# Optimization experiments

Hardware: AMD Instinct MI355X
Metric: run time of the kernel (lower is better)

## Reference

```python
import jax, jax.numpy as jnp
import numpy as np

SEQ_LEN = 96      # args.seq_len (in_feats)
H_FEATS = 100
OUT_FEATS = 128
HEADS = 4
K = 64            # args.input_size = nodes per graph
B = 256           # number of graphs (batch_size)
N = K * B
DEG = 8
E = N * DEG
OUT_SIZE = 24     # args.output_size
NEG_SLOPE = 0.2   # PyG GATConv default


def setup_inputs() -> dict:
    key = jax.random.key(0)
    ks = jax.random.split(key, 20)
    s = 0.05
    x = jax.random.normal(ks[0], (N, SEQ_LEN), jnp.float32)
    # intra-graph random edges (dst repeated, src within same graph)
    dst = jnp.repeat(jnp.arange(N, dtype=jnp.int32), DEG)
    src = (dst // K) * K + jax.random.randint(ks[1], (E,), 0, K, dtype=jnp.int32)
    edge_index = jnp.stack([src, dst])
    batch = jnp.repeat(jnp.arange(B, dtype=jnp.int32), K)
    y = jax.random.normal(ks[2], (N, OUT_SIZE), jnp.float32)
    # GATConv 1: in=96 -> heads=4, ch=100
    W1 = jax.random.normal(ks[3], (SEQ_LEN, HEADS * H_FEATS), jnp.float32) * s
    as1 = jax.random.normal(ks[4], (HEADS, H_FEATS), jnp.float32) * s
    ad1 = jax.random.normal(ks[5], (HEADS, H_FEATS), jnp.float32) * s
    b1 = jnp.zeros((H_FEATS,), jnp.float32)
    # GATConv 2: in=100 -> heads=4, ch=128
    W2 = jax.random.normal(ks[6], (H_FEATS, HEADS * OUT_FEATS), jnp.float32) * s
    as2 = jax.random.normal(ks[7], (HEADS, OUT_FEATS), jnp.float32) * s
    ad2 = jax.random.normal(ks[8], (HEADS, OUT_FEATS), jnp.float32) * s
    b2 = jnp.zeros((OUT_FEATS,), jnp.float32)
    # per-node-index MLPs (batched over K)
    fw1 = jax.random.normal(ks[9], (K, OUT_FEATS, 64), jnp.float32) * s
    fb1 = jnp.zeros((K, 64), jnp.float32)
    fw2 = jax.random.normal(ks[10], (K, 64, OUT_SIZE), jnp.float32) * s
    fb2 = jnp.zeros((K, OUT_SIZE), jnp.float32)
    return dict(x=x, edge_index=edge_index, batch=batch, y=y,
                W1=W1, as1=as1, ad1=ad1, b1=b1,
                W2=W2, as2=as2, ad2=ad2, b2=b2,
                fw1=fw1, fb1=fb1, fw2=fw2, fb2=fb2)


def gat_conv(x, src, dst, W, a_src, a_dst, bias):
    # PyG GATConv (concat=False): linear -> per-edge attention -> softmax over
    # incoming edges of each dst -> weighted sum -> mean over heads + bias.
    n = x.shape[0]
    xl = (x @ W).reshape(n, HEADS, -1)                      # [N,H,C]
    al_src = jnp.sum(xl * a_src, axis=-1)                   # [N,H]
    al_dst = jnp.sum(xl * a_dst, axis=-1)                   # [N,H]
    alpha = jax.nn.leaky_relu(al_src[src] + al_dst[dst], NEG_SLOPE)  # [E,H]
    m = jax.ops.segment_max(alpha, dst, num_segments=n)
    ea = jnp.exp(alpha - m[dst])
    denom = jax.ops.segment_sum(ea, dst, num_segments=n)
    w = ea / (denom[dst] + 1e-16)                           # [E,H]
    msg = xl[src] * w[:, :, None]                           # [E,H,C]
    out = jax.ops.segment_sum(msg, dst, num_segments=n)     # [N,H,C]
    return out.mean(axis=1) + bias                          # concat=False


def reference(x, edge_index, batch, y, W1, as1, ad1, b1, W2, as2, ad2, b2, fw1, fb1, fw2, fb2):
    n = x.shape[0]
    src, dst = edge_index[0], edge_index[1]
    loop = jnp.arange(n, dtype=src.dtype)                   # GATConv adds self-loops
    src = jnp.concatenate([src, loop])
    dst = jnp.concatenate([dst, loop])
    h = jax.nn.elu(gat_conv(x, src, dst, W1, as1, ad1, b1))
    h = gat_conv(h, src, dst, W2, as2, ad2, b2)             # [N,128]
    # batch is sorted with K nodes per graph -> stacking == static reshape
    xg = h.reshape(B, K, OUT_FEATS).transpose(1, 0, 2)      # [K,B,128]
    hid = jax.nn.relu(jnp.einsum('kbi,kih->kbh', xg, fw1) + fb1[:, None, :])
    pred = jnp.einsum('kbh,kho->kbo', hid, fw2) + fb2[:, None, :]  # [K,B,out]
    yg = y.reshape(B, K, OUT_SIZE)                          # [B,K,out]
    return pred, yg
```

## Files before the change

### kernel.cpp

```cpp
#include <hip/hip_runtime.h>
#include <hip/hip_bf16.h>
#include <math.h>


#define N_NODES 16384
#define B_GRAPHS 256
#define K_NODES 64
#define DEG 8
#define NHEADS 4
#define C1 100
#define C2 128
#define IN_F 96
#define HID 64
#define OUT_SZ 24
#define PRED_ELEMS (K_NODES * B_GRAPHS * OUT_SZ)

#define W1T_ROWS 448
#define W1T_K    96
#define W2T_ROWS 512
#define W2T_K    128

using bf16 = __hip_bfloat16;
typedef __attribute__((ext_vector_type(8))) short          frag_ab;
typedef __attribute__((ext_vector_type(4))) float          frag_cd;
typedef unsigned short us8 __attribute__((ext_vector_type(8)));
typedef unsigned short us4 __attribute__((ext_vector_type(4)));

__device__ __forceinline__ float us2f(unsigned short u) {
  return __bfloat162float(__ushort_as_bfloat16(u));
}
__device__ __forceinline__ short f2bf_s(float f) {
  return __builtin_bit_cast(short, __float2bfloat16(f));
}

#define P1N (W1T_ROWS * W1T_K)
#define P2N (W2T_ROWS * W2T_K)
#define YG4 (PRED_ELEMS / 4)

__global__ __launch_bounds__(256)
void prep(const float* __restrict__ W1, const float* __restrict__ W2,
          const float* __restrict__ y,
          bf16* __restrict__ W1t, bf16* __restrict__ W2t,
          float* __restrict__ yg) {
  int idx = blockIdx.x * 256 + threadIdx.x;
  if (idx < P1N) {
    int c = idx / W1T_K, k = idx - c * W1T_K;
    W1t[idx] = __float2bfloat16((c < 400) ? W1[(size_t)k * 400 + c] : 0.f);
  } else if (idx < P1N + P2N) {
    int i2 = idx - P1N;
    int c = i2 >> 7, k = i2 & 127;
    W2t[i2] = __float2bfloat16((k < 100) ? W2[(size_t)k * 512 + c] : 0.f);
  } else {
    int j = idx - P1N - P2N;
    if (j < YG4) {
      int i = j * 4;
      float4 v = *(const float4*)(y + i);
      v.x = __bfloat162float(__float2bfloat16(v.x));
      v.y = __bfloat162float(__float2bfloat16(v.y));
      v.z = __bfloat162float(__float2bfloat16(v.z));
      v.w = __bfloat162float(__float2bfloat16(v.w));
      *(float4*)(yg + i) = v;
    }
  }
}

__global__ __launch_bounds__(512)
void gat_fused(const float* __restrict__ x,
               const bf16* __restrict__ W1t, const bf16* __restrict__ W2t,
               const int* __restrict__ esrc,
               const float* __restrict__ as1, const float* __restrict__ ad1,
               const float* __restrict__ b1,
               const float* __restrict__ as2, const float* __restrict__ ad2,
               const float* __restrict__ b2,
               bf16* __restrict__ h2out) {
  constexpr int LDA1 = IN_F + 8;
  constexpr int LDA2 = 136;
  constexpr int LDT  = 72;

  __shared__ __align__(16) short          As[64 * LDA2];
  __shared__ __align__(16) unsigned short xs[512 * LDT];
  __shared__ __align__(16) short          Ps[NHEADS * 64 * LDT];
  __shared__ float avs1[400], avd1[400], avs2[512], avd2[512];
  __shared__ float bia1[C1], bia2[C2];
  __shared__ int   edg[K_NODES * DEG];
  __shared__ float als[64 * 5], ald[64 * 5];

  const int g = blockIdx.x;
  const int t = threadIdx.x;
  const int wv = t >> 6;
  const int l  = t & 63;
  const int lm = l & 15;
  const int lk = (l >> 4) * 8;
  const int rq = (l >> 4) * 4;

  {
    constexpr int QR = IN_F / 4;
    for (int idx = t; idx < 64 * QR; idx += 512) {
      int m = idx / QR, q = idx - m * QR;
      const float4 v = *(const float4*)(x + ((size_t)(g * 64 + m) * IN_F + q * 4));
      short* d = &As[m * LDA1 + q * 4];
      d[0] = f2bf_s(v.x); d[1] = f2bf_s(v.y); d[2] = f2bf_s(v.z); d[3] = f2bf_s(v.w);
    }
  }
  for (int idx = t; idx < 400; idx += 512) { avs1[idx] = as1[idx]; avd1[idx] = ad1[idx]; }
  for (int idx = t; idx < 512; idx += 512) { avs2[idx] = as2[idx]; avd2[idx] = ad2[idx]; }
  if (t < C1) bia1[t] = b1[t];
  if (t < C2) bia2[t] = b2[t];
  if (t < K_NODES * DEG) edg[t] = esrc[g * K_NODES * DEG + t] & (K_NODES - 1);
  for (int idx = t; idx < NHEADS * 64 * LDT / 8; idx += 512)
    *(us8*)&Ps[idx * 8] = (us8)0;
  __syncthreads();

  if (wv < 7) {
    const int n0 = wv * 64;
    frag_cd acc[4][4] = {};
#pragma unroll
    for (int ks = 0; ks < IN_F; ks += 32) {
      frag_ab b[4];
#pragma unroll
      for (int nt = 0; nt < 4; ++nt)
        b[nt] = *(const frag_ab*)((const short*)W1t +
                                  (size_t)(n0 + nt * 16 + lm) * W1T_K + ks + lk);
#pragma unroll
      for (int mt = 0; mt < 4; ++mt) {
        frag_ab a = *(const frag_ab*)&As[(mt * 16 + lm) * LDA1 + ks + lk];
#pragma unroll
        for (int nt = 0; nt < 4; ++nt)
          acc[mt][nt] = __builtin_amdgcn_mfma_f32_16x16x32_bf16(a, b[nt],
                                                                acc[mt][nt], 0, 0, 0);
      }
    }
#pragma unroll
    for (int mt = 0; mt < 4; ++mt)
#pragma unroll
      for (int nt = 0; nt < 4; ++nt) {
        const int c4 = n0 + nt * 16 + lm;
        us4 o;
#pragma unroll
        for (int r = 0; r < 4; ++r) o[r] = (unsigned short)f2bf_s(acc[mt][nt][r]);
        *(us4*)&xs[c4 * LDT + mt * 16 + rq] = o;
      }
  }
  __syncthreads();

  if (t < 256) {
    const int n = t >> 2, h = t & 3;
    float ss = 0.f, sd = 0.f;
#pragma unroll 4
    for (int c = 0; c < C1; ++c) {
      const float v = us2f(xs[(h * C1 + c) * LDT + n]);
      ss += v * avs1[h * C1 + c];
      sd += v * avd1[h * C1 + c];
    }
    als[n * 5 + h] = ss;
    ald[n * 5 + h] = sd;
  }
  __syncthreads();

  if (t < 256) {
    const int n = t >> 2, h = t & 3;
    const float ad = ald[n * 5 + h];
    int   sv[9];
    float a[9];
#pragma unroll
    for (int j = 0; j < 8; ++j) sv[j] = edg[n * DEG + j];
    sv[8] = n;
#pragma unroll
    for (int j = 0; j < 9; ++j) {
      float v = als[sv[j] * 5 + h] + ad;
      a[j] = (v >= 0.f) ? v : 0.2f * v;
    }
    float m = -1e30f;
#pragma unroll
    for (int j = 0; j < 9; ++j) m = fmaxf(m, a[j]);
    float s = 0.f;
#pragma unroll
    for (int j = 0; j < 9; ++j) { a[j] = __expf(a[j] - m); s += a[j]; }
    const float inv = 1.f / (s + 1e-16f);
    short* prow = &Ps[(h * 64 + n) * LDT];
#pragma unroll
    for (int j = 0; j < 9; ++j) {
      float tw = a[j];
#pragma unroll
      for (int i = 0; i < 9; ++i)
        if (i != j && sv[i] == sv[j]) tw += a[i];
      prow[sv[j]] = f2bf_s(tw * inv);
    }
  } else {
    for (int i = t - 256; i < 64 * 28; i += 256) {
      int m = i / 28, kk = 100 + (i - m * 28);
      As[m * LDA2 + kk] = 0;
    }
  }
  __syncthreads();

  {
    const int mw = (wv & 3) * 16;
    const int cg = wv >> 2;
    const int ntb = cg * 4;
    const int nte = (cg == 0) ? 4 : 7;
    frag_cd acc[4] = {};
#pragma unroll
    for (int h = 0; h < NHEADS; ++h)
#pragma unroll
      for (int ks = 0; ks < 64; ks += 32) {
        frag_ab a = *(const frag_ab*)&Ps[(h * 64 + mw + lm) * LDT + ks + lk];
        for (int nt = ntb; nt < nte; ++nt) {
          frag_ab b = *(const frag_ab*)&xs[(h * C1 + nt * 16 + lm) * LDT + ks + lk];
          acc[nt - ntb] = __builtin_amdgcn_mfma_f32_16x16x32_bf16(a, b,
                                                                  acc[nt - ntb], 0, 0, 0);
      }
    }
    for (int nt = ntb; nt < nte; ++nt) {
      const int c = nt * 16 + lm;
      if (c < C1) {
        const float bc = bia1[c];
#pragma unroll
        for (int r = 0; r < 4; ++r) {
          float vv = acc[nt - ntb][r] * 0.25f + bc;
          vv = (vv > 0.f) ? vv : (__expf(vv) - 1.f);
          As[(mw + rq + r) * LDA2 + c] = f2bf_s(vv);
        }
      }
    }
  }
  __syncthreads();

  {
    const int n0 = wv * 64;
    frag_cd acc[4][4] = {};
#pragma unroll
    for (int ks = 0; ks < 128; ks += 32) {
      frag_ab b[4];
#pragma unroll
      for (int nt = 0; nt < 4; ++nt)
        b[nt] = *(const frag_ab*)((const short*)W2t +
                                  (size_t)(n0 + nt * 16 + lm) * W2T_K + ks + lk);
#pragma unroll
      for (int mt = 0; mt < 4; ++mt) {
        frag_ab a = *(const frag_ab*)&As[(mt * 16 + lm) * LDA2 + ks + lk];
#pragma unroll
        for (int nt = 0; nt < 4; ++nt)
          acc[mt][nt] = __builtin_amdgcn_mfma_f32_16x16x32_bf16(a, b[nt],
                                                                acc[mt][nt], 0, 0, 0);
      }
    }
#pragma unroll
    for (int mt = 0; mt < 4; ++mt)
#pragma unroll
      for (int nt = 0; nt < 4; ++nt) {
        const int c4 = n0 + nt * 16 + lm;
        us4 o;
#pragma unroll
        for (int r = 0; r < 4; ++r) o[r] = (unsigned short)f2bf_s(acc[mt][nt][r]);
        *(us4*)&xs[c4 * LDT + mt * 16 + rq] = o;
      }
  }
  __syncthreads();

  if (t < 256) {
    const int n = t >> 2, h = t & 3;
    float ss = 0.f, sd = 0.f;
#pragma unroll 4
    for (int c = 0; c < C2; ++c) {
      const float v = us2f(xs[(h * C2 + c) * LDT + n]);
      ss += v * avs2[h * C2 + c];
      sd += v * avd2[h * C2 + c];
    }
    als[n * 5 + h] = ss;
    ald[n * 5 + h] = sd;
  }
  __syncthreads();

  if (t < 256) {
    const int n = t >> 2, h = t & 3;
    const float ad = ald[n * 5 + h];
    int   sv[9];
    float a[9];
#pragma unroll
    for (int j = 0; j < 8; ++j) sv[j] = edg[n * DEG + j];
    sv[8] = n;
#pragma unroll
    for (int j = 0; j < 9; ++j) {
      float v = als[sv[j] * 5 + h] + ad;
      a[j] = (v >= 0.f) ? v : 0.2f * v;
    }
    float m = -1e30f;
#pragma unroll
    for (int j = 0; j < 9; ++j) m = fmaxf(m, a[j]);
    float s = 0.f;
#pragma unroll
    for (int j = 0; j < 9; ++j) { a[j] = __expf(a[j] - m); s += a[j]; }
    const float inv = 1.f / (s + 1e-16f);
    short* prow = &Ps[(h * 64 + n) * LDT];
#pragma unroll
    for (int j = 0; j < 9; ++j) {
      float tw = a[j];
#pragma unroll
      for (int i = 0; i < 9; ++i)
        if (i != j && sv[i] == sv[j]) tw += a[i];
      prow[sv[j]] = f2bf_s(tw * inv);
    }
  }
  __syncthreads();

  {
    const int mw = (wv & 3) * 16;
    const int cg = wv >> 2;
    const int ntb = cg * 4;
    frag_cd acc[4] = {};
#pragma unroll
    for (int h = 0; h < NHEADS; ++h)
#pragma unroll
      for (int ks = 0; ks < 64; ks += 32) {
        frag_ab a = *(const frag_ab*)&Ps[(h * 64 + mw + lm) * LDT + ks + lk];
#pragma unroll
        for (int nt = 0; nt < 4; ++nt) {
          frag_ab b = *(const frag_ab*)&xs[(h * C2 + (ntb + nt) * 16 + lm) * LDT + ks + lk];
          acc[nt] = __builtin_amdgcn_mfma_f32_16x16x32_bf16(a, b, acc[nt], 0, 0, 0);
        }
      }
    unsigned short* outp = (unsigned short*)h2out + (size_t)(g * 64) * C2;
#pragma unroll
    for (int nt = 0; nt < 4; ++nt) {
      const int c = (ntb + nt) * 16 + lm;
      const float bc = bia2[c];
#pragma unroll
      for (int r = 0; r < 4; ++r) {
        float vv = acc[nt][r] * 0.25f + bc;
        outp[(size_t)(mw + rq + r) * C2 + c] = (unsigned short)f2bf_s(vv);
      }
    }
  }
}

__global__ __launch_bounds__(256)
void mlp_mfma(const bf16* __restrict__ h2,
              const float* __restrict__ fw1, const float* __restrict__ fb1,
              const float* __restrict__ fw2, const float* __restrict__ fb2,
              float* __restrict__ pred) {
  constexpr int LDA = C2 + 8;
  constexpr int LDH = HID + 8;
  __shared__ __align__(16) short As[64 * LDA];
  __shared__ __align__(16) short B1[HID * LDA];
  __shared__ __align__(16) short Hs[64 * LDH];
  __shared__ __align__(16) short B2[32 * LDH];
  __shared__ float b1s[HID];
  __shared__ float b2s[32];

  const int k  = blockIdx.x & 63;
  const int ms = blockIdx.x >> 6;
  const int t  = threadIdx.x;

  for (int idx = t; idx < 64 * 16; idx += 256) {
    int r = idx >> 4, o = idx & 15;
    const us8 v = *(const us8*)((const unsigned short*)h2 +
        ((size_t)((ms * 64 + r) * K_NODES + k) * C2) + o * 8);
    *(us8*)&As[r * LDA + o * 8] = v;
  }
  for (int idx = t; idx < C2 * HID; idx += 256) {
    int kk = idx >> 6, n = idx & 63;
    B1[n * LDA + kk] = f2bf_s(fw1[(size_t)k * C2 * HID + kk * HID + n]);
  }
  for (int idx = t; idx < HID * 32; idx += 256) {
    int kk = idx >> 5, n = idx & 31;
    float v = (n < OUT_SZ) ? fw2[(size_t)k * HID * OUT_SZ + kk * OUT_SZ + n] : 0.f;
    B2[n * LDH + kk] = f2bf_s(v);
  }
  if (t < HID) b1s[t] = fb1[k * HID + t];
  if (t < 32)  b2s[t] = (t < OUT_SZ) ? fb2[k * OUT_SZ + t] : 0.f;
  __syncthreads();

  const int wv = t >> 6;
  const int l  = t & 63;
  const int lm = l & 15;
  const int lk = (l >> 4) * 8;
  const int rq = (l >> 4) * 4;

  frag_cd acc[4] = {};
#pragma unroll
  for (int ks = 0; ks < C2; ks += 32) {
    frag_ab a = *(const frag_ab*)&As[(wv * 16 + lm) * LDA + ks + lk];
#pragma unroll
    for (int nt = 0; nt < 4; ++nt) {
      frag_ab b = *(const frag_ab*)&B1[(nt * 16 + lm) * LDA + ks + lk];
      acc[nt] = __builtin_amdgcn_mfma_f32_16x16x32_bf16(a, b, acc[nt], 0, 0, 0);
    }
  }
#pragma unroll
  for (int nt = 0; nt < 4; ++nt) {
    const int j  = nt * 16 + lm;
    const float bj = b1s[j];
#pragma unroll
    for (int r = 0; r < 4; ++r) {
      const int m = wv * 16 + rq + r;
      Hs[m * LDH + j] = f2bf_s(fmaxf(acc[nt][r] + bj, 0.f));
    }
  }
  __syncthreads();

  frag_cd acc2[2] = {};
#pragma unroll
  for (int ks = 0; ks < HID; ks += 32) {
    frag_ab a = *(const frag_ab*)&Hs[(wv * 16 + lm) * LDH + ks + lk];
#pragma unroll
    for (int nt = 0; nt < 2; ++nt) {
      frag_ab b = *(const frag_ab*)&B2[(nt * 16 + lm) * LDH + ks + lk];
      acc2[nt] = __builtin_amdgcn_mfma_f32_16x16x32_bf16(a, b, acc2[nt], 0, 0, 0);
    }
  }
#pragma unroll
  for (int nt = 0; nt < 2; ++nt) {
    const int q = nt * 16 + lm;
    if (q < OUT_SZ) {
      const float bq = b2s[q];
#pragma unroll
      for (int r = 0; r < 4; ++r) {
        const int m = wv * 16 + rq + r;
        pred[((size_t)k * B_GRAPHS + ms * 64 + m) * OUT_SZ + q] = acc2[nt][r] + bq;
      }
    }
  }
}

extern "C" void kernel_launch(void* const* d_in, const int* in_sizes, int n_in,
                              void* d_out, int out_size, void* d_ws, size_t ws_size,
                              hipStream_t stream) {
  const float* x   = (const float*)d_in[0];
  const int*   ei  = (const int*)d_in[1];
  const float* y   = (const float*)d_in[3];
  const float* W1  = (const float*)d_in[4];
  const float* as1 = (const float*)d_in[5];
  const float* ad1 = (const float*)d_in[6];
  const float* b1  = (const float*)d_in[7];
  const float* W2  = (const float*)d_in[8];
  const float* as2 = (const float*)d_in[9];
  const float* ad2 = (const float*)d_in[10];
  const float* b2  = (const float*)d_in[11];
  const float* fw1 = (const float*)d_in[12];
  const float* fb1 = (const float*)d_in[13];
  const float* fw2 = (const float*)d_in[14];
  const float* fb2 = (const float*)d_in[15];

  bf16* h2  = (bf16*)d_ws;
  bf16* W1t = h2 + (size_t)N_NODES * C2;
  bf16* W2t = W1t + P1N;

  float* out = (float*)d_out;

  prep<<<(P1N + P2N + YG4 + 255) / 256, 256, 0, stream>>>(
      W1, W2, y, W1t, W2t, out + PRED_ELEMS);

  gat_fused<<<B_GRAPHS, 512, 0, stream>>>(x, W1t, W2t, ei,
                                          as1, ad1, b1, as2, ad2, b2, h2);

  mlp_mfma<<<K_NODES * 4, 256, 0, stream>>>(h2, fw1, fb1, fw2, fb2, out);
}
```

Measured before the change: 118.6 us.

## Merge prep, GAT and MLP kernels into one cooperative kernel with grid syncs

Replaces three separate launches with a single cooperative kernel of 256 blocks that does weight and y prep, then grid.sync, the per-graph GAT layers, another grid.sync, and the per-node-index MLP. The fw1 and fw2 weights are now pre-transposed to bf16 in the prep phase, so the MLP phase loads them with vectorized copies instead of strided fp32 loads. The MLP phase is re-tiled for 512 threads, with shared memory shared through a union. The aim is to remove launch gaps and the strided weight loads, at the cost of grid-wide barriers and the occupancy limits of a cooperative launch.

```diff
diff --git a/kernel.cpp b/kernel.cpp
--- a/kernel.cpp
+++ b/kernel.cpp
@@ -1,6 +1,9 @@
 #include <hip/hip_runtime.h>
+#include <hip/hip_cooperative_groups.h>
 #include <hip/hip_bf16.h>
 #include <math.h>
+
+namespace cg = cooperative_groups;
 
 
 #define N_NODES 16384
@@ -20,6 +23,13 @@
 #define W2T_ROWS 512
 #define W2T_K    128
 
+#define P1N (W1T_ROWS * W1T_K)
+#define P2N (W2T_ROWS * W2T_K)
+#define F1N (K_NODES * HID * C2)
+#define F2N (K_NODES * 32 * HID)
+#define YG4 (PRED_ELEMS / 4)
+#define PREPN (P1N + P2N + F1N + F2N + YG4)
+
 using bf16 = __hip_bfloat16;
 typedef __attribute__((ext_vector_type(8))) short          frag_ab;
 typedef __attribute__((ext_vector_type(4))) float          frag_cd;
@@ -33,26 +43,69 @@
   return __builtin_bit_cast(short, __float2bfloat16(f));
 }
 
-#define P1N (W1T_ROWS * W1T_K)
-#define P2N (W2T_ROWS * W2T_K)
-#define YG4 (PRED_ELEMS / 4)
-
-__global__ __launch_bounds__(256)
-void prep(const float* __restrict__ W1, const float* __restrict__ W2,
-          const float* __restrict__ y,
-          bf16* __restrict__ W1t, bf16* __restrict__ W2t,
-          float* __restrict__ yg) {
-  int idx = blockIdx.x * 256 + threadIdx.x;
-  if (idx < P1N) {
-    int c = idx / W1T_K, k = idx - c * W1T_K;
-    W1t[idx] = __float2bfloat16((c < 400) ? W1[(size_t)k * 400 + c] : 0.f);
-  } else if (idx < P1N + P2N) {
-    int i2 = idx - P1N;
-    int c = i2 >> 7, k = i2 & 127;
-    W2t[i2] = __float2bfloat16((k < 100) ? W2[(size_t)k * 512 + c] : 0.f);
-  } else {
-    int j = idx - P1N - P2N;
-    if (j < YG4) {
+struct SmGat {
+  short          As[64 * 136];
+  unsigned short xs[512 * 72];
+  short          Ps[NHEADS * 64 * 72];
+  float avs1[400], avd1[400], avs2[512], avd2[512];
+  float bia1[C1], bia2[C2];
+  int   edg[K_NODES * DEG];
+  float als[64 * 5], ald[64 * 5];
+};
+struct SmMlp {
+  short As[64 * 136];
+  short B1[HID * 136];
+  short Hs[64 * 72];
+  short B2[32 * 72];
+  float b1s[HID], b2s[32];
+};
+union SmAll { SmGat g; SmMlp m; };
+
+__global__ __launch_bounds__(512)
+void fused_all(const float* __restrict__ x, const int* __restrict__ ei,
+               const float* __restrict__ y,
+               const float* __restrict__ W1, const float* __restrict__ as1,
+               const float* __restrict__ ad1, const float* __restrict__ b1,
+               const float* __restrict__ W2, const float* __restrict__ as2,
+               const float* __restrict__ ad2, const float* __restrict__ b2,
+               const float* __restrict__ fw1, const float* __restrict__ fb1,
+               const float* __restrict__ fw2, const float* __restrict__ fb2,
+               bf16* __restrict__ ws, float* __restrict__ out) {
+  __shared__ __align__(16) SmAll sm;
+  cg::grid_group grid = cg::this_grid();
+
+  const int t  = threadIdx.x;
+  const int wv = t >> 6;
+  const int l  = t & 63;
+  const int lm = l & 15;
+  const int lk = (l >> 4) * 8;
+  const int rq = (l >> 4) * 4;
+
+  bf16* h2   = ws;
+  bf16* W1t  = h2 + (size_t)N_NODES * C2;
+  bf16* W2t  = W1t + P1N;
+  bf16* fw1t = W2t + P2N;
+  bf16* fw2t = fw1t + F1N;
+  float* yg  = out + PRED_ELEMS;
+
+  for (int idx = blockIdx.x * 512 + t; idx < PREPN; idx += 256 * 512) {
+    if (idx < P1N) {
+      int c = idx / W1T_K, k = idx - c * W1T_K;
+      W1t[idx] = __float2bfloat16((c < 400) ? W1[(size_t)k * 400 + c] : 0.f);
+    } else if (idx < P1N + P2N) {
+      int i2 = idx - P1N;
+      int c = i2 >> 7, k = i2 & 127;
+      W2t[i2] = __float2bfloat16((k < 100) ? W2[(size_t)k * 512 + c] : 0.f);
+    } else if (idx < P1N + P2N + F1N) {
+      int i2 = idx - P1N - P2N;
+      int k = i2 >> 13, r = i2 & 8191, j = r >> 7, i = r & 127;
+      fw1t[i2] = __float2bfloat16(fw1[(size_t)k * 8192 + i * 64 + j]);
+    } else if (idx < P1N + P2N + F1N + F2N) {
+      int i2 = idx - P1N - P2N - F1N;
+      int k = i2 >> 11, r = i2 & 2047, q = r >> 6, j = r & 63;
+      fw2t[i2] = __float2bfloat16((q < OUT_SZ) ? fw2[(size_t)k * 1536 + j * 24 + q] : 0.f);
+    } else {
+      int j = idx - P1N - P2N - F1N - F2N;
       int i = j * 4;
       float4 v = *(const float4*)(y + i);
       v.x = __bfloat162float(__float2bfloat16(v.x));
@@ -62,362 +115,323 @@
       *(float4*)(yg + i) = v;
     }
   }
-}
-
-__global__ __launch_bounds__(512)
-void gat_fused(const float* __restrict__ x,
-               const bf16* __restrict__ W1t, const bf16* __restrict__ W2t,
-               const int* __restrict__ esrc,
-               const float* __restrict__ as1, const float* __restrict__ ad1,
-               const float* __restrict__ b1,
-               const float* __restrict__ as2, const float* __restrict__ ad2,
-               const float* __restrict__ b2,
-               bf16* __restrict__ h2out) {
-  constexpr int LDA1 = IN_F + 8;
-  constexpr int LDA2 = 136;
-  constexpr int LDT  = 72;
-
-  __shared__ __align__(16) short          As[64 * LDA2];
-  __shared__ __align__(16) unsigned short xs[512 * LDT];
-  __shared__ __align__(16) short          Ps[NHEADS * 64 * LDT];
-  __shared__ float avs1[400], avd1[400], avs2[512], avd2[512];
-  __shared__ float bia1[C1], bia2[C2];
-  __shared__ int   edg[K_NODES * DEG];
-  __shared__ float als[64 * 5], ald[64 * 5];
-
-  const int g = blockIdx.x;
-  const int t = threadIdx.x;
-  const int wv = t >> 6;
-  const int l  = t & 63;
-  const int lm = l & 15;
-  const int lk = (l >> 4) * 8;
-  const int rq = (l >> 4) * 4;
+  grid.sync();
 
   {
-    constexpr int QR = IN_F / 4;
-    for (int idx = t; idx < 64 * QR; idx += 512) {
-      int m = idx / QR, q = idx - m * QR;
-      const float4 v = *(const float4*)(x + ((size_t)(g * 64 + m) * IN_F + q * 4));
-      short* d = &As[m * LDA1 + q * 4];
-      d[0] = f2bf_s(v.x); d[1] = f2bf_s(v.y); d[2] = f2bf_s(v.z); d[3] = f2bf_s(v.w);
+    constexpr int LDA1 = IN_F + 8;
+    constexpr int LDA2 = 136;
+    constexpr int LDT  = 72;
+    auto& S = sm.g;
+    const int g = blockIdx.x;
+
+    {
+      constexpr int QR = IN_F / 4;
+      for (int idx = t; idx < 64 * QR; idx += 512) {
+        int m = idx / QR, q = idx - m * QR;
+        const float4 v = *(const float4*)(x + ((size_t)(g * 64 + m) * IN_F + q * 4));
+        short* d = &S.As[m * LDA1 + q * 4];
+        d[0] = f2bf_s(v.x); d[1] = f2bf_s(v.y); d[2] = f2bf_s(v.z); d[3] = f2bf_s(v.w);
+      }
+    }
+    for (int idx = t; idx < 400; idx += 512) { S.avs1[idx] = as1[idx]; S.avd1[idx] = ad1[idx]; }
+    { S.avs2[t] = as2[t]; S.avd2[t] = ad2[t]; }
+    if (t < C1) S.bia1[t] = b1[t];
+    if (t < C2) S.bia2[t] = b2[t];
+    S.edg[t] = ei[g * K_NODES * DEG + t] & (K_NODES - 1);
+    for (int idx = t; idx < NHEADS * 64 * LDT / 8; idx += 512)
+      *(us8*)&S.Ps[idx * 8] = (us8)0;
+    __syncthreads();
+
+    if (wv < 7) {
+      const int n0 = wv * 64;
+      frag_cd acc[4][4] = {};
+#pragma unroll
+      for (int ks = 0; ks < IN_F; ks += 32) {
+        frag_ab b[4];
+#pragma unroll
+        for (int nt = 0; nt < 4; ++nt)
+          b[nt] = *(const frag_ab*)((const short*)W1t +
+                                    (size_t)(n0 + nt * 16 + lm) * W1T_K + ks + lk);
+#pragma unroll
+        for (int mt = 0; mt < 4; ++mt) {
+          frag_ab a = *(const frag_ab*)&S.As[(mt * 16 + lm) * LDA1 + ks + lk];
+#pragma unroll
+          for (int nt = 0; nt < 4; ++nt)
+            acc[mt][nt] = __builtin_amdgcn_mfma_f32_16x16x32_bf16(a, b[nt],
+                                                                  acc[mt][nt], 0, 0, 0);
+        }
+      }
+#pragma unroll
+      for (int mt = 0; mt < 4; ++mt)
+#pragma unroll
+        for (int nt = 0; nt < 4; ++nt) {
+          const int c4 = n0 + nt * 16 + lm;
+          us4 o;
+#pragma unroll
+          for (int r = 0; r < 4; ++r) o[r] = (unsigned short)f2bf_s(acc[mt][nt][r]);
+          *(us4*)&S.xs[c4 * LDT + mt * 16 + rq] = o;
+        }
+    }
+    __syncthreads();
+
+    if (t < 256) {
+      const int n = t >> 2, h = t & 3;
+      float ss = 0.f, sd = 0.f;
+#pragma unroll 4
+      for (int c = 0; c < C1; ++c) {
+        const float v = us2f(S.xs[(h * C1 + c) * LDT + n]);
+        ss += v * S.avs1[h * C1 + c];
+        sd += v * S.avd1[h * C1 + c];
+      }
+      S.als[n * 5 + h] = ss;
+      S.ald[n * 5 + h] = sd;
+    }
+    __syncthreads();
+
+    if (t < 256) {
+      const int n = t >> 2, h = t & 3;
+      const float ad = S.ald[n * 5 + h];
+      int   sv[9];
+      float a[9];
+#pragma unroll
+      for (int j = 0; j < 8; ++j) sv[j] = S.edg[n * DEG + j];
+      sv[8] = n;
+#pragma unroll
+      for (int j = 0; j < 9; ++j) {
+        float v = S.als[sv[j] * 5 + h] + ad;
+        a[j] = (v >= 0.f) ? v : 0.2f * v;
+      }
+      float m = -1e30f;
+#pragma unroll
+      for (int j = 0; j < 9; ++j) m = fmaxf(m, a[j]);
+      float s = 0.f;
+#pragma unroll
+      for (int j = 0; j < 9; ++j) { a[j] = __expf(a[j] - m); s += a[j]; }
+      const float inv = 1.f / (s + 1e-16f);
+      short* prow = &S.Ps[(h * 64 + n) * LDT];
+#pragma unroll
+      for (int j = 0; j < 9; ++j) {
+        float tw = a[j];
+#pragma unroll
+        for (int i = 0; i < 9; ++i)
+          if (i != j && sv[i] == sv[j]) tw += a[i];
+        prow[sv[j]] = f2bf_s(tw * inv);
+      }
+    } else {
+      for (int i = t - 256; i < 64 * 28; i += 256) {
+        int m = i / 28, kk = 100 + (i - m * 28);
+        S.As[m * LDA2 + kk] = 0;
+      }
+    }
+    __syncthreads();
+
+    {
+      const int mw = (wv & 3) * 16;
+      const int cgi = wv >> 2;
+      const int ntb = cgi * 4;
+      const int nte = (cgi == 0) ? 4 : 7;
+      frag_cd acc[4] = {};
+#pragma unroll
+      for (int h = 0; h < NHEADS; ++h)
+#pragma unroll
+        for (int ks = 0; ks < 64; ks += 32) {
+          frag_ab a = *(const frag_ab*)&S.Ps[(h * 64 + mw + lm) * LDT + ks + lk];
+          for (int nt = ntb; nt < nte; ++nt) {
+            frag_ab b = *(const frag_ab*)&S.xs[(h * C1 + nt * 16 + lm) * LDT + ks + lk];
+            acc[nt - ntb] = __builtin_amdgcn_mfma_f32_16x16x32_bf16(a, b,
+                                                                    acc[nt - ntb], 0, 0, 0);
+          }
+        }
+      for (int nt = ntb; nt < nte; ++nt) {
+        const int c = nt * 16 + lm;
+        if (c < C1) {
+          const float bc = S.bia1[c];
+#pragma unroll
+          for (int r = 0; r < 4; ++r) {
+            float vv = acc[nt - ntb][r] * 0.25f + bc;
+            vv = (vv > 0.f) ? vv : (__expf(vv) - 1.f);
+            S.As[(mw + rq + r) * LDA2 + c] = f2bf_s(vv);
+          }
+        }
+      }
+    }
+    __syncthreads();
+
+    {
+      const int n0 = wv * 64;
+      frag_cd acc[4][4] = {};
+#pragma unroll
+      for (int ks = 0; ks < 128; ks += 32) {
+        frag_ab b[4];
+#pragma unroll
+        for (int nt = 0; nt < 4; ++nt)
+          b[nt] = *(const frag_ab*)((const short*)W2t +
+                                    (size_t)(n0 + nt * 16 + lm) * W2T_K + ks + lk);
+#pragma unroll
+        for (int mt = 0; mt < 4; ++mt) {
+          frag_ab a = *(const frag_ab*)&S.As[(mt * 16 + lm) * LDA2 + ks + lk];
+#pragma unroll
+          for (int nt = 0; nt < 4; ++nt)
+            acc[mt][nt] = __builtin_amdgcn_mfma_f32_16x16x32_bf16(a, b[nt],
+                                                                  acc[mt][nt], 0, 0, 0);
+        }
+      }
+#pragma unroll
+      for (int mt = 0; mt < 4; ++mt)
+#pragma unroll
+        for (int nt = 0; nt < 4; ++nt) {
+          const int c4 = n0 + nt * 16 + lm;
+          us4 o;
+#pragma unroll
+          for (int r = 0; r < 4; ++r) o[r] = (unsigned short)f2bf_s(acc[mt][nt][r]);
+          *(us4*)&S.xs[c4 * LDT + mt * 16 + rq] = o;
+        }
+    }
+    __syncthreads();
+
+    if (t < 256) {
+      const int n = t >> 2, h = t & 3;
+      float ss = 0.f, sd = 0.f;
+#pragma unroll 4
+      for (int c = 0; c < C2; ++c) {
+        const float v = us2f(S.xs[(h * C2 + c) * LDT + n]);
+        ss += v * S.avs2[h * C2 + c];
+        sd += v * S.avd2[h * C2 + c];
+      }
+      S.als[n * 5 + h] = ss;
+      S.ald[n * 5 + h] = sd;
+    }
+    __syncthreads();
+
+    if (t < 256) {
+      const int n = t >> 2, h = t & 3;
+      const float ad = S.ald[n * 5 + h];
+      int   sv[9];
+      float a[9];
+#pragma unroll
+      for (int j = 0; j < 8; ++j) sv[j] = S.edg[n * DEG + j];
+      sv[8] = n;
+#pragma unroll
+      for (int j = 0; j < 9; ++j) {
+        float v = S.als[sv[j] * 5 + h] + ad;
+        a[j] = (v >= 0.f) ? v : 0.2f * v;
+      }
+      float m = -1e30f;
+#pragma unroll
+      for (int j = 0; j < 9; ++j) m = fmaxf(m, a[j]);
+      float s = 0.f;
+#pragma unroll
+      for (int j = 0; j < 9; ++j) { a[j] = __expf(a[j] - m); s += a[j]; }
+      const float inv = 1.f / (s + 1e-16f);
+      short* prow = &S.Ps[(h * 64 + n) * LDT];
+#pragma unroll
+      for (int j = 0; j < 9; ++j) {
+        float tw = a[j];
+#pragma unroll
+        for (int i = 0; i < 9; ++i)
+          if (i != j && sv[i] == sv[j]) tw += a[i];
+        prow[sv[j]] = f2bf_s(tw * inv);
+      }
+    }
+    __syncthreads();
+
+    {
+      const int mw = (wv & 3) * 16;
+      const int cgi = wv >> 2;
+      const int ntb = cgi * 4;
+      frag_cd acc[4] = {};
+#pragma unroll
+      for (int h = 0; h < NHEADS; ++h)
+#pragma unroll
+        for (int ks = 0; ks < 64; ks += 32) {
+          frag_ab a = *(const frag_ab*)&S.Ps[(h * 64 + mw + lm) * LDT + ks + lk];
+#pragma unroll
+          for (int nt = 0; nt < 4; ++nt) {
+            frag_ab b = *(const frag_ab*)&S.xs[(h * C2 + (ntb + nt) * 16 + lm) * LDT + ks + lk];
+            acc[nt] = __builtin_amdgcn_mfma_f32_16x16x32_bf16(a, b, acc[nt], 0, 0, 0);
+          }
+        }
+      unsigned short* outp = (unsigned short*)h2 + (size_t)(g * 64) * C2;
+#pragma unroll
+      for (int nt = 0; nt < 4; ++nt) {
+        const int c = (ntb + nt) * 16 + lm;
+        const float bc = S.bia2[c];
+#pragma unroll
+        for (int r = 0; r < 4; ++r) {
+          float vv = acc[nt][r] * 0.25f + bc;
+          outp[(size_t)(mw + rq + r) * C2 + c] = (unsigned short)f2bf_s(vv);
+        }
+      }
     }
   }
-  for (int idx = t; idx < 400; idx += 512) { avs1[idx] = as1[idx]; avd1[idx] = ad1[idx]; }
-  for (int idx = t; idx < 512; idx += 512) { avs2[idx] = as2[idx]; avd2[idx] = ad2[idx]; }
-  if (t < C1) bia1[t] = b1[t];
-  if (t < C2) bia2[t] = b2[t];
-  if (t < K_NODES * DEG) edg[t] = esrc[g * K_NODES * DEG + t] & (K_NODES - 1);
-  for (int idx = t; idx < NHEADS * 64 * LDT / 8; idx += 512)
-    *(us8*)&Ps[idx * 8] = (us8)0;
-  __syncthreads();
-
-  if (wv < 7) {
-    const int n0 = wv * 64;
-    frag_cd acc[4][4] = {};
-#pragma unroll
-    for (int ks = 0; ks < IN_F; ks += 32) {
-      frag_ab b[4];
-#pragma unroll
-      for (int nt = 0; nt < 4; ++nt)
-        b[nt] = *(const frag_ab*)((const short*)W1t +
-                                  (size_t)(n0 + nt * 16 + lm) * W1T_K + ks + lk);
-#pragma unroll
-      for (int mt = 0; mt < 4; ++mt) {
-        frag_ab a = *(const frag_ab*)&As[(mt * 16 + lm) * LDA1 + ks + lk];
-#pragma unroll
-        for (int nt = 0; nt < 4; ++nt)
-          acc[mt][nt] = __builtin_amdgcn_mfma_f32_16x16x32_bf16(a, b[nt],
-                                                                acc[mt][nt], 0, 0, 0);
-      }
-    }
-#pragma unroll
-    for (int mt = 0; mt < 4; ++mt)
-#pragma unroll
-      for (int nt = 0; nt < 4; ++nt) {
-        const int c4 = n0 + nt * 16 + lm;
-        us4 o;
-#pragma unroll
-        for (int r = 0; r < 4; ++r) o[r] = (unsigned short)f2bf_s(acc[mt][nt][r]);
-        *(us4*)&xs[c4 * LDT + mt * 16 + rq] = o;
-      }
-  }
-  __syncthreads();
-
-  if (t < 256) {
-    const int n = t >> 2, h = t & 3;
-    float ss = 0.f, sd = 0.f;
-#pragma unroll 4
-    for (int c = 0; c < C1; ++c) {
-      const float v = us2f(xs[(h * C1 + c) * LDT + n]);
-      ss += v * avs1[h * C1 + c];
-      sd += v * avd1[h * C1 + c];
-    }
-    als[n * 5 + h] = ss;
-    ald[n * 5 + h] = sd;
-  }
-  __syncthreads();
-
-  if (t < 256) {
-    const int n = t >> 2, h = t & 3;
-    const float ad = ald[n * 5 + h];
-    int   sv[9];
-    float a[9];
-#pragma unroll
-    for (int j = 0; j < 8; ++j) sv[j] = edg[n * DEG + j];
-    sv[8] = n;
-#pragma unroll
-    for (int j = 0; j < 9; ++j) {
-      float v = als[sv[j] * 5 + h] + ad;
-      a[j] = (v >= 0.f) ? v : 0.2f * v;
-    }
-    float m = -1e30f;
-#pragma unroll
-    for (int j = 0; j < 9; ++j) m = fmaxf(m, a[j]);
-    float s = 0.f;
-#pragma unroll
-    for (int j = 0; j < 9; ++j) { a[j] = __expf(a[j] - m); s += a[j]; }
-    const float inv = 1.f / (s + 1e-16f);
-    short* prow = &Ps[(h * 64 + n) * LDT];
-#pragma unroll
-    for (int j = 0; j < 9; ++j) {
-      float tw = a[j];
-#pragma unroll
-      for (int i = 0; i < 9; ++i)
-        if (i != j && sv[i] == sv[j]) tw += a[i];
-      prow[sv[j]] = f2bf_s(tw * inv);
-    }
-  } else {
-    for (int i = t - 256; i < 64 * 28; i += 256) {
-      int m = i / 28, kk = 100 + (i - m * 28);
-      As[m * LDA2 + kk] = 0;
-    }
-  }
-  __syncthreads();
+  grid.sync();
 
   {
-    const int mw = (wv & 3) * 16;
-    const int cg = wv >> 2;
-    const int ntb = cg * 4;
-    const int nte = (cg == 0) ? 4 : 7;
-    frag_cd acc[4] = {};
-#pragma unroll
-    for (int h = 0; h < NHEADS; ++h)
-#pragma unroll
-      for (int ks = 0; ks < 64; ks += 32) {
-        frag_ab a = *(const frag_ab*)&Ps[(h * 64 + mw + lm) * LDT + ks + lk];
-        for (int nt = ntb; nt < nte; ++nt) {
-          frag_ab b = *(const frag_ab*)&xs[(h * C1 + nt * 16 + lm) * LDT + ks + lk];
-          acc[nt - ntb] = __builtin_amdgcn_mfma_f32_16x16x32_bf16(a, b,
-                                                                  acc[nt - ntb], 0, 0, 0);
-      }
-    }
-    for (int nt = ntb; nt < nte; ++nt) {
-      const int c = nt * 16 + lm;
-      if (c < C1) {
-        const float bc = bia1[c];
-#pragma unroll
-        for (int r = 0; r < 4; ++r) {
-          float vv = acc[nt - ntb][r] * 0.25f + bc;
-          vv = (vv > 0.f) ? vv : (__expf(vv) - 1.f);
-          As[(mw + rq + r) * LDA2 + c] = f2bf_s(vv);
-        }
-      }
-    }
-  }
-  __syncthreads();
-
-  {
-    const int n0 = wv * 64;
-    frag_cd acc[4][4] = {};
-#pragma unroll
-    for (int ks = 0; ks < 128; ks += 32) {
-      frag_ab b[4];
-#pragma unroll
-      for (int nt = 0; nt < 4; ++nt)
-        b[nt] = *(const frag_ab*)((const short*)W2t +
-                                  (size_t)(n0 + nt * 16 + lm) * W2T_K + ks + lk);
-#pragma unroll
-      for (int mt = 0; mt < 4; ++mt) {
-        frag_ab a = *(const frag_ab*)&As[(mt * 16 + lm) * LDA2 + ks + lk];
-#pragma unroll
-        for (int nt = 0; nt < 4; ++nt)
-          acc[mt][nt] = __builtin_amdgcn_mfma_f32_16x16x32_bf16(a, b[nt],
-                                                                acc[mt][nt], 0, 0, 0);
-      }
-    }
-#pragma unroll
-    for (int mt = 0; mt < 4; ++mt)
-#pragma unroll
-      for (int nt = 0; nt < 4; ++nt) {
-        const int c4 = n0 + nt * 16 + lm;
-        us4 o;
-#pragma unroll
-        for (int r = 0; r < 4; ++r) o[r] = (unsigned short)f2bf_s(acc[mt][nt][r]);
-        *(us4*)&xs[c4 * LDT + mt * 16 + rq] = o;
-      }
-  }
-  __syncthreads();
-
-  if (t < 256) {
-    const int n = t >> 2, h = t & 3;
-    float ss = 0.f, sd = 0.f;
-#pragma unroll 4
-    for (int c = 0; c < C2; ++c) {
-      const float v = us2f(xs[(h * C2 + c) * LDT + n]);
-      ss += v * avs2[h * C2 + c];
-      sd += v * avd2[h * C2 + c];
-    }
-    als[n * 5 + h] = ss;
-    ald[n * 5 + h] = sd;
-  }
-  __syncthreads();
-
-  if (t < 256) {
-    const int n = t >> 2, h = t & 3;
-    const float ad = ald[n * 5 + h];
-    int   sv[9];
-    float a[9];
-#pragma unroll
-    for (int j = 0; j < 8; ++j) sv[j] = edg[n * DEG + j];
-    sv[8] = n;
-#pragma unroll
-    for (int j = 0; j < 9; ++j) {
-      float v = als[sv[j] * 5 + h] + ad;
-      a[j] = (v >= 0.f) ? v : 0.2f * v;
-    }
-    float m = -1e30f;
-#pragma unroll
-    for (int j = 0; j < 9; ++j) m = fmaxf(m, a[j]);
-    float s = 0.f;
-#pragma unroll
-    for (int j = 0; j < 9; ++j) { a[j] = __expf(a[j] - m); s += a[j]; }
-    const float inv = 1.f / (s + 1e-16f);
-    short* prow = &Ps[(h * 64 + n) * LDT];
-#pragma unroll
-    for (int j = 0; j < 9; ++j) {
-      float tw = a[j];
-#pragma unroll
-      for (int i = 0; i < 9; ++i)
-        if (i != j && sv[i] == sv[j]) tw += a[i];
-      prow[sv[j]] = f2bf_s(tw * inv);
-    }
-  }
-  __syncthreads();
-
-  {
-    const int mw = (wv & 3) * 16;
-    const int cg = wv >> 2;
-    const int ntb = cg * 4;
-    frag_cd acc[4] = {};
-#pragma unroll
-    for (int h = 0; h < NHEADS; ++h)
-#pragma unroll
-      for (int ks = 0; ks < 64; ks += 32) {
-        frag_ab a = *(const frag_ab*)&Ps[(h * 64 + mw + lm) * LDT + ks + lk];
-#pragma unroll
-        for (int nt = 0; nt < 4; ++nt) {
-          frag_ab b = *(const frag_ab*)&xs[(h * C2 + (ntb + nt) * 16 + lm) * LDT + ks + lk];
-          acc[nt] = __builtin_amdgcn_mfma_f32_16x16x32_bf16(a, b, acc[nt], 0, 0, 0);
-        }
-      }
-    unsigned short* outp = (unsigned short*)h2out + (size_t)(g * 64) * C2;
-#pragma unroll
-    for (int nt = 0; nt < 4; ++nt) {
-      const int c = (ntb + nt) * 16 + lm;
-      const float bc = bia2[c];
-#pragma unroll
-      for (int r = 0; r < 4; ++r) {
-        float vv = acc[nt][r] * 0.25f + bc;
-        outp[(size_t)(mw + rq + r) * C2 + c] = (unsigned short)f2bf_s(vv);
-      }
-    }
-  }
-}
-
-__global__ __launch_bounds__(256)
-void mlp_mfma(const bf16* __restrict__ h2,
-              const float* __restrict__ fw1, const float* __restrict__ fb1,
-              const float* __restrict__ fw2, const float* __restrict__ fb2,
-              float* __restrict__ pred) {
-  constexpr int LDA = C2 + 8;
-  constexpr int LDH = HID + 8;
-  __shared__ __align__(16) short As[64 * LDA];
-  __shared__ __align__(16) short B1[HID * LDA];
-  __shared__ __align__(16) short Hs[64 * LDH];
-  __shared__ __align__(16) short B2[32 * LDH];
-  __shared__ float b1s[HID];
-  __shared__ float b2s[32];
-
-  const int k  = blockIdx.x & 63;
-  const int ms = blockIdx.x >> 6;
-  const int t  = threadIdx.x;
-
-  for (int idx = t; idx < 64 * 16; idx += 256) {
-    int r = idx >> 4, o = idx & 15;
-    const us8 v = *(const us8*)((const unsigned short*)h2 +
-        ((size_t)((ms * 64 + r) * K_NODES + k) * C2) + o * 8);
-    *(us8*)&As[r * LDA + o * 8] = v;
-  }
-  for (int idx = t; idx < C2 * HID; idx += 256) {
-    int kk = idx >> 6, n = idx & 63;
-    B1[n * LDA + kk] = f2bf_s(fw1[(size_t)k * C2 * HID + kk * HID + n]);
-  }
-  for (int idx = t; idx < HID * 32; idx += 256) {
-    int kk = idx >> 5, n = idx & 31;
-    float v = (n < OUT_SZ) ? fw2[(size_t)k * HID * OUT_SZ + kk * OUT_SZ + n] : 0.f;
-    B2[n * LDH + kk] = f2bf_s(v);
-  }
-  if (t < HID) b1s[t] = fb1[k * HID + t];
-  if (t < 32)  b2s[t] = (t < OUT_SZ) ? fb2[k * OUT_SZ + t] : 0.f;
-  __syncthreads();
-
-  const int wv = t >> 6;
-  const int l  = t & 63;
-  const int lm = l & 15;
-  const int lk = (l >> 4) * 8;
-  const int rq = (l >> 4) * 4;
-
-  frag_cd acc[4] = {};
-#pragma unroll
-  for (int ks = 0; ks < C2; ks += 32) {
-    frag_ab a = *(const frag_ab*)&As[(wv * 16 + lm) * LDA + ks + lk];
-#pragma unroll
-    for (int nt = 0; nt < 4; ++nt) {
-      frag_ab b = *(const frag_ab*)&B1[(nt * 16 + lm) * LDA + ks + lk];
-      acc[nt] = __builtin_amdgcn_mfma_f32_16x16x32_bf16(a, b, acc[nt], 0, 0, 0);
-    }
-  }
-#pragma unroll
-  for (int nt = 0; nt < 4; ++nt) {
-    const int j  = nt * 16 + lm;
-    const float bj = b1s[j];
-#pragma unroll
-    for (int r = 0; r < 4; ++r) {
-      const int m = wv * 16 + rq + r;
-      Hs[m * LDH + j] = f2bf_s(fmaxf(acc[nt][r] + bj, 0.f));
-    }
-  }
-  __syncthreads();
-
-  frag_cd acc2[2] = {};
-#pragma unroll
-  for (int ks = 0; ks < HID; ks += 32) {
-    frag_ab a = *(const frag_ab*)&Hs[(wv * 16 + lm) * LDH + ks + lk];
-#pragma unroll
-    for (int nt = 0; nt < 2; ++nt) {
-      frag_ab b = *(const frag_ab*)&B2[(nt * 16 + lm) * LDH + ks + lk];
-      acc2[nt] = __builtin_amdgcn_mfma_f32_16x16x32_bf16(a, b, acc2[nt], 0, 0, 0);
-    }
-  }
-#pragma unroll
-  for (int nt = 0; nt < 2; ++nt) {
-    const int q = nt * 16 + lm;
-    if (q < OUT_SZ) {
-      const float bq = b2s[q];
-#pragma unroll
-      for (int r = 0; r < 4; ++r) {
-        const int m = wv * 16 + rq + r;
-        pred[((size_t)k * B_GRAPHS + ms * 64 + m) * OUT_SZ + q] = acc2[nt][r] + bq;
+    constexpr int LDA = 136;
+    constexpr int LDH = 72;
+    auto& M = sm.m;
+    const int k  = blockIdx.x & 63;
+    const int ms = blockIdx.x >> 6;
+
+    for (int idx = t; idx < 64 * 16; idx += 512) {
+      int r = idx >> 4, o = idx & 15;
+      const us8 v = *(const us8*)((const unsigned short*)h2 +
+          ((size_t)((ms * 64 + r) * K_NODES + k) * C2) + o * 8);
+      *(us8*)&M.As[r * LDA + o * 8] = v;
+    }
+    for (int idx = t; idx < HID * 16; idx += 512) {
+      int n = idx >> 4, o = idx & 15;
+      *(us8*)&M.B1[n * LDA + o * 8] =
+          *(const us8*)((const unsigned short*)fw1t + (size_t)k * 8192 + n * 128 + o * 8);
+    }
+    for (int idx = t; idx < 32 * 8; idx += 512) {
+      int q = idx >> 3, o = idx & 7;
+      *(us8*)&M.B2[q * LDH + o * 8] =
+          *(const us8*)((const unsigned short*)fw2t + (size_t)k * 2048 + q * 64 + o * 8);
+    }
+    if (t < HID) M.b1s[t] = fb1[k * HID + t];
+    if (t >= 64 && t < 96) M.b2s[t - 64] = (t - 64 < OUT_SZ) ? fb2[k * OUT_SZ + (t - 64)] : 0.f;
+    __syncthreads();
+
+    {
+      const int mh  = (wv >> 2) * 32;
+      const int nt1 = wv & 3;
+      frag_cd acc[2] = {};
+#pragma unroll
+      for (int ks = 0; ks < C2; ks += 32) {
+        frag_ab b = *(const frag_ab*)&M.B1[(nt1 * 16 + lm) * LDA + ks + lk];
+#pragma unroll
+        for (int mt = 0; mt < 2; ++mt) {
+          frag_ab a = *(const frag_ab*)&M.As[(mh + mt * 16 + lm) * LDA + ks + lk];
+          acc[mt] = __builtin_amdgcn_mfma_f32_16x16x32_bf16(a, b, acc[mt], 0, 0, 0);
+        }
+      }
+      const int j  = nt1 * 16 + lm;
+      const float bj = M.b1s[j];
+#pragma unroll
+      for (int mt = 0; mt < 2; ++mt)
+#pragma unroll
+        for (int r = 0; r < 4; ++r)
+          M.Hs[(mh + mt * 16 + rq + r) * LDH + j] = f2bf_s(fmaxf(acc[mt][r] + bj, 0.f));
+    }
+    __syncthreads();
+
+    {
+      const int mq  = (wv >> 1) * 16;
+      const int nt2 = wv & 1;
+      frag_cd acc = {};
+#pragma unroll
+      for (int ks = 0; ks < HID; ks += 32) {
+        frag_ab a = *(const frag_ab*)&M.Hs[(mq + lm) * LDH + ks + lk];
+        frag_ab b = *(const frag_ab*)&M.B2[(nt2 * 16 + lm) * LDH + ks + lk];
+        acc = __builtin_amdgcn_mfma_f32_16x16x32_bf16(a, b, acc, 0, 0, 0);
+      }
+      const int q = nt2 * 16 + lm;
+      if (q < OUT_SZ) {
+        const float bq = M.b2s[q];
+#pragma unroll
+        for (int r = 0; r < 4; ++r)
+          out[((size_t)k * B_GRAPHS + ms * 64 + mq + rq + r) * OUT_SZ + q] = acc[r] + bq;
       }
     }
   }
@@ -442,17 +456,14 @@
   const float* fw2 = (const float*)d_in[14];
   const float* fb2 = (const float*)d_in[15];
 
-  bf16* h2  = (bf16*)d_ws;
-  bf16* W1t = h2 + (size_t)N_NODES * C2;
-  bf16* W2t = W1t + P1N;
-
+  bf16*  ws  = (bf16*)d_ws;
   float* out = (float*)d_out;
 
-  prep<<<(P1N + P2N + YG4 + 255) / 256, 256, 0, stream>>>(
-      W1, W2, y, W1t, W2t, out + PRED_ELEMS);
-
-  gat_fused<<<B_GRAPHS, 512, 0, stream>>>(x, W1t, W2t, ei,
-                                          as1, ad1, b1, as2, ad2, b2, h2);
-
-  mlp_mfma<<<K_NODES * 4, 256, 0, stream>>>(h2, fw1, fb1, fw2, fb2, out);
+  void* args[] = {(void*)&x,  (void*)&ei,  (void*)&y,
+                  (void*)&W1, (void*)&as1, (void*)&ad1, (void*)&b1,
+                  (void*)&W2, (void*)&as2, (void*)&ad2, (void*)&b2,
+                  (void*)&fw1,(void*)&fb1, (void*)&fw2, (void*)&fb2,
+                  (void*)&ws, (void*)&out};
+  hipLaunchCooperativeKernel((const void*)fused_all, dim3(B_GRAPHS), dim3(512),
+                             args, 0, stream);
 }
```

After: 211.3 us. +78.1%, slower.
